# Performance work log

Measured on AMD Instinct MI355X. Metric: run time of the kernel, lower is better.

The kernel has to match this reference:

```python
import jax, jax.numpy as jnp
import numpy as np

B, D, M, H = 1024, 2048, 32, 32


def setup_inputs() -> dict:
    key = jax.random.key(0)
    k1, k2, k3, k4, k5 = jax.random.split(key, 5)
    pre_act_history = jax.random.normal(k1, (B, D, M), dtype=jnp.float32)
    # kaiming_uniform-ish scale for weights
    w1 = jax.random.normal(k2, (D, H, M), dtype=jnp.float32) * (1.0 / np.sqrt(M))
    b1 = jax.random.normal(k3, (D, H), dtype=jnp.float32) * 0.01
    w_out = jax.random.normal(k4, (D, 1, H), dtype=jnp.float32) * (1.0 / np.sqrt(H))
    b_out = jax.random.normal(k5, (D,), dtype=jnp.float32) * 0.01
    return {"pre_act_history": pre_act_history, "w1": w1, "b1": b1,
            "w_out": w_out, "b_out": b_out}


def reference(pre_act_history, w1, b1, w_out, b_out):
    # Per-neuron first layer: (B,D,M) x (D,H,M) -> (B,D,H)
    x = jnp.einsum('bdm,dhm->bdh', pre_act_history, w1) + b1
    x = jax.nn.gelu(x, approximate=False)  # torch F.gelu default is exact erf
    # nlm_depth == 2 -> mid is Identity
    # Per-neuron output layer: (B,D,H) x (D,1,H) -> (B,D,1)
    out = jnp.einsum('bdh,doh->bdo', x, w_out) + b_out[:, None]
    return jnp.tanh(out[..., 0])  # (B, D)
```

## Files before the change

kernel.cpp:

```cpp
#include <hip/hip_runtime.h>
#include <math.h>

#define B_ 1024
#define D_ 2048
#define M_ 32
#define H_ 32

#define DPB 8
#define BPB 128
#define OPAD 9

typedef _Float16 f16x8 __attribute__((ext_vector_type(8)));
typedef float    f32x4 __attribute__((ext_vector_type(4)));

__device__ __forceinline__ float fast_erff(float x) {
    float ax = fabsf(x);
    float t  = __builtin_amdgcn_rcpf(1.0f + 0.3275911f * ax);
    float p  = 1.061405429f;
    p = p * t - 1.453152027f;
    p = p * t + 1.421413741f;
    p = p * t - 0.284496736f;
    p = p * t + 0.254829592f;
    float e = __expf(-ax * ax);
    float r = 1.0f - p * t * e;
    return copysignf(r, x);
}

__device__ __forceinline__ float gelu_exact(float x) {
    return 0.5f * x * (1.0f + fast_erff(x * 0.70710678118f));
}

__device__ __forceinline__ float fast_tanhf(float x) {
    return 1.0f - 2.0f * __builtin_amdgcn_rcpf(__expf(2.0f * x) + 1.0f);
}

__device__ __forceinline__ f16x8 cvt8(const float4 a, const float4 b) {
    f16x8 v;
    v[0] = (_Float16)a.x; v[1] = (_Float16)a.y; v[2] = (_Float16)a.z; v[3] = (_Float16)a.w;
    v[4] = (_Float16)b.x; v[5] = (_Float16)b.y; v[6] = (_Float16)b.z; v[7] = (_Float16)b.w;
    return v;
}

__global__ __launch_bounds__(512)
void nlm_kernel(const float* __restrict__ pre,
                const float* __restrict__ w1,
                const float* __restrict__ b1,
                const float* __restrict__ w_out,
                const float* __restrict__ b_out,
                float* __restrict__ out) {
    __shared__ float obuf[BPB * OPAD];

    const int tid  = threadIdx.x;
    const int lane = tid & 63;
    const int w    = tid >> 6;
    const int c16  = lane & 15;
    const int g    = lane >> 4;

    const int linear = ((blockIdx.x & 7) << 8) | (blockIdx.x >> 3);
    const int dt = linear & 255;
    const int bt = linear >> 8;
    const int d0 = dt * DPB;
    const int b0 = bt * BPB;

    const int du = __builtin_amdgcn_readfirstlane(d0 + w);

    const float* wbase = w1 + (size_t)du * (H_ * M_);
    const f16x8 wa0 = cvt8(*(const float4*)(wbase + c16 * M_ + g * 8),
                           *(const float4*)(wbase + c16 * M_ + g * 8 + 4));
    const f16x8 wa1 = cvt8(*(const float4*)(wbase + (c16 + 16) * M_ + g * 8),
                           *(const float4*)(wbase + (c16 + 16) * M_ + g * 8 + 4));

    const f32x4 b1q0 = *(const f32x4*)(b1    + (size_t)du * H_ + g * 4);
    const f32x4 b1q1 = *(const f32x4*)(b1    + (size_t)du * H_ + g * 4 + 16);
    const f32x4 woq0 = *(const f32x4*)(w_out + (size_t)du * H_ + g * 4);
    const f32x4 woq1 = *(const f32x4*)(w_out + (size_t)du * H_ + g * 4 + 16);
    const float bo   = b_out[du];

    const float* pbase = pre + ((size_t)(b0 + c16) * D_ + du) * M_ + g * 8;

#pragma unroll 2
    for (int t = 0; t < 8; ++t) {
        const float* pa = pbase + (size_t)t * 16 * D_ * M_;
        const f16x8 pf = cvt8(*(const float4*)(pa), *(const float4*)(pa + 4));

        f32x4 acc0 = b1q0, acc1 = b1q1;
        acc0 = __builtin_amdgcn_mfma_f32_16x16x32_f16(wa0, pf, acc0, 0, 0, 0);
        acc1 = __builtin_amdgcn_mfma_f32_16x16x32_f16(wa1, pf, acc1, 0, 0, 0);

        float p = 0.f;
#pragma unroll
        for (int r = 0; r < 4; ++r) {
            p = fmaf(gelu_exact(acc0[r]), woq0[r], p);
            p = fmaf(gelu_exact(acc1[r]), woq1[r], p);
        }
        p += __shfl_xor(p, 16, 64);
        p += __shfl_xor(p, 32, 64);

        if (lane < 16)
            obuf[(t * 16 + c16) * OPAD + w] = fast_tanhf(p + bo);
    }

    __syncthreads();

    if (tid < 2 * BPB) {
        const int r  = tid >> 1;
        const int cc = (tid & 1) * 4;
        float4 o;
        o.x = obuf[r * OPAD + cc + 0];
        o.y = obuf[r * OPAD + cc + 1];
        o.z = obuf[r * OPAD + cc + 2];
        o.w = obuf[r * OPAD + cc + 3];
        *reinterpret_cast<float4*>(out + (size_t)(b0 + r) * D_ + d0 + cc) = o;
    }
}

extern "C" void kernel_launch(void* const* d_in, const int* in_sizes, int n_in,
                              void* d_out, int out_size, void* d_ws, size_t ws_size,
                              hipStream_t stream) {
    const float* pre   = (const float*)d_in[0];
    const float* w1    = (const float*)d_in[1];
    const float* b1    = (const float*)d_in[2];
    const float* w_out = (const float*)d_in[3];
    const float* b_out = (const float*)d_in[4];
    float* out = (float*)d_out;

    const int grid = (D_ / DPB) * (B_ / BPB);
    nlm_kernel<<<dim3(grid), dim3(512), 0, stream>>>(pre, w1, b1, w_out, b_out, out);
}
```

Before: 58.24 us.

## Double-buffer activation tiles via global_load_lds and pack f16 conversion

```diff
diff --git a/kernel.cpp b/kernel.cpp
--- a/kernel.cpp
+++ b/kernel.cpp
@@ -8,9 +8,13 @@
 
 #define DPB 8
 #define BPB 128
+#define NT  8
 #define OPAD 9
 
 typedef _Float16 f16x8 __attribute__((ext_vector_type(8)));
+typedef __fp16   h16x2 __attribute__((ext_vector_type(2)));
+typedef __fp16   h16x4 __attribute__((ext_vector_type(4)));
+typedef __fp16   h16x8 __attribute__((ext_vector_type(8)));
 typedef float    f32x4 __attribute__((ext_vector_type(4)));
 
 __device__ __forceinline__ float fast_erff(float x) {
@@ -35,10 +39,20 @@
 }
 
 __device__ __forceinline__ f16x8 cvt8(const float4 a, const float4 b) {
-    f16x8 v;
-    v[0] = (_Float16)a.x; v[1] = (_Float16)a.y; v[2] = (_Float16)a.z; v[3] = (_Float16)a.w;
-    v[4] = (_Float16)b.x; v[5] = (_Float16)b.y; v[6] = (_Float16)b.z; v[7] = (_Float16)b.w;
-    return v;
+    const h16x2 h0 = __builtin_amdgcn_cvt_pkrtz(a.x, a.y);
+    const h16x2 h1 = __builtin_amdgcn_cvt_pkrtz(a.z, a.w);
+    const h16x2 h2 = __builtin_amdgcn_cvt_pkrtz(b.x, b.y);
+    const h16x2 h3 = __builtin_amdgcn_cvt_pkrtz(b.z, b.w);
+    const h16x4 lo = __builtin_shufflevector(h0, h1, 0, 1, 2, 3);
+    const h16x4 hi = __builtin_shufflevector(h2, h3, 0, 1, 2, 3);
+    const h16x8 v  = __builtin_shufflevector(lo, hi, 0, 1, 2, 3, 4, 5, 6, 7);
+    return __builtin_bit_cast(f16x8, v);
+}
+
+typedef __attribute__((address_space(1))) const unsigned int ga_u32;
+typedef __attribute__((address_space(3))) unsigned int ls_u32;
+__device__ __forceinline__ void gload_lds16(const float* g, float* l) {
+    __builtin_amdgcn_global_load_lds((ga_u32*)g, (ls_u32*)l, 16, 0, 0);
 }
 
 __global__ __launch_bounds__(512)
@@ -48,6 +62,7 @@
                 const float* __restrict__ w_out,
                 const float* __restrict__ b_out,
                 float* __restrict__ out) {
+    __shared__ float pbuf[2][16 * 256];
     __shared__ float obuf[BPB * OPAD];
 
     const int tid  = threadIdx.x;
@@ -76,12 +91,29 @@
     const f32x4 woq1 = *(const f32x4*)(w_out + (size_t)du * H_ + g * 4 + 16);
     const float bo   = b_out[du];
 
-    const float* pbase = pre + ((size_t)(b0 + c16) * D_ + du) * M_ + g * 8;
+#define STAGE(T, BUFI)                                                          \
+    {                                                                           \
+        const float* g0_ = pre + ((size_t)(b0 + (T) * 16 + 2 * w) * D_ + d0) * M_; \
+        const float* g1_ = g0_ + (size_t)D_ * M_;                               \
+        gload_lds16(g0_ + lane * 4, &pbuf[BUFI][(2 * w) * 256]);                \
+        gload_lds16(g1_ + lane * 4, &pbuf[BUFI][(2 * w + 1) * 256]);            \
+    }
 
-#pragma unroll 2
-    for (int t = 0; t < 8; ++t) {
-        const float* pa = pbase + (size_t)t * 16 * D_ * M_;
-        const f16x8 pf = cvt8(*(const float4*)(pa), *(const float4*)(pa + 4));
+    STAGE(0, 0)
+    __syncthreads();
+
+#pragma unroll
+    for (int t = 0; t < NT; ++t) {
+        const int cur = t & 1;
+
+        if (t + 1 < NT) {
+            if ((t + 1) & 1) { STAGE(t + 1, 1) } else { STAGE(t + 1, 0) }
+        }
+
+        const float4* prd = reinterpret_cast<const float4*>(&pbuf[cur][0]);
+        const float4 lo = prd[c16 * 64 + w * 8 + g * 2];
+        const float4 hi = prd[c16 * 64 + w * 8 + g * 2 + 1];
+        const f16x8 pf = cvt8(lo, hi);
 
         f32x4 acc0 = b1q0, acc1 = b1q1;
         acc0 = __builtin_amdgcn_mfma_f32_16x16x32_f16(wa0, pf, acc0, 0, 0, 0);
@@ -98,9 +130,9 @@
 
         if (lane < 16)
             obuf[(t * 16 + c16) * OPAD + w] = fast_tanhf(p + bo);
+
+        __syncthreads();
     }
-
-    __syncthreads();
 
     if (tid < 2 * BPB) {
         const int r  = tid >> 1;
```

Result: slower. 63.06 us (+8.3%).
